# Performance work log

Hardware: AMD Instinct MI355X
Metric: run time of the kernel (lower is better)

Reference implementation:

```python
import jax, jax.numpy as jnp
import numpy as np

EMBD_DIM = 512
HIDDEN_DIM = 512
TARGET_DIM = 128
BATCH = 64
MAX_SET = 2048


def setup_inputs() -> dict:
    key = jax.random.key(0)
    ks = jax.random.split(key, 10)
    E, H, T = EMBD_DIM, HIDDEN_DIM, TARGET_DIM
    s = lambda fan_in: 1.0 / np.sqrt(fan_in)
    return {
        "words": jax.random.normal(ks[0], (BATCH, MAX_SET, E), dtype=jnp.float32),
        # attention_layer: Linear(2E -> H) followed by tanh; v: (H, 1)
        "W_att": jax.random.uniform(ks[1], (2 * E, H), jnp.float32, -s(2 * E), s(2 * E)),
        "b_att": jax.random.uniform(ks[2], (H,), jnp.float32, -s(2 * E), s(2 * E)),
        "v": jax.random.normal(ks[3], (H, 1), dtype=jnp.float32),
        # pred_net: Linear(E,H) -> ReLU -> Linear(H,H) -> ReLU -> Linear(H,T)
        "W1": jax.random.uniform(ks[4], (E, H), jnp.float32, -s(E), s(E)),
        "b1": jax.random.uniform(ks[5], (H,), jnp.float32, -s(E), s(E)),
        "W2": jax.random.uniform(ks[6], (H, H), jnp.float32, -s(H), s(H)),
        "b2": jax.random.uniform(ks[7], (H,), jnp.float32, -s(H), s(H)),
        "W3": jax.random.uniform(ks[8], (H, T), jnp.float32, -s(H), s(H)),
        "b3": jax.random.uniform(ks[9], (T,), jnp.float32, -s(H), s(H)),
    }


def reference(words, W_att, b_att, v, W1, b1, W2, b2, W3, b3):
    # words: [B, S, E]. A row is "valid" iff its feature-sum is nonzero
    # (matches words.sum(2).abs().sign() in the torch code).
    mask = jnp.sign(jnp.abs(words.sum(-1)))           # [B, S], 0/1 float
    lengths = mask.sum(axis=1, keepdims=True)          # [B, 1]
    # context = mean over valid rows (padded rows are exactly zero)
    context = words.sum(axis=1, keepdims=True) / lengths[..., None]  # [B, 1, E]
    context = jnp.broadcast_to(context, words.shape)   # [B, S, E]

    x = jnp.concatenate([words, context], axis=-1)     # [B, S, 2E]
    h = jnp.tanh(x @ W_att + b_att)                    # [B, S, H]
    scores = (h @ v)[..., 0]                           # [B, S]

    # per-segment softmax over valid rows only (masked_select + per-batch
    # Softmax in the original == masked softmax here)
    scores = jnp.where(mask > 0, scores, jnp.full_like(scores, -1e30))
    attn = jax.nn.softmax(scores, axis=1)              # [B, S]

    rep = jnp.einsum("bs,bse->be", attn, words)        # [B, E]

    pred = jax.nn.relu(rep @ W1 + b1)
    pred = jax.nn.relu(pred @ W2 + b2)
    pred = pred @ W3 + b3                              # [B, T]
    return pred
```

## Files before the change

### kernel.cpp

```cpp
#include <hip/hip_runtime.h>
#include <hip/hip_bf16.h>
#include <hip/hip_fp16.h>
#include <math.h>

#define B 64
#define S 2048
#define E 512
#define HD 512
#define TD 128
#define M_TOT (B*S)

#define OFF_MASK   0
#define OFF_CTXP   (OFF_MASK + B*S)
#define OFF_LENP   (OFF_CTXP + 8*B*E)
#define OFF_CB     (OFF_LENP + 8*B)
#define OFF_REPP   (OFF_CB + B*HD)
#define OFF_SC     (OFF_REPP + 8*B*E)
#define OFF_WPK    (OFF_SC + B*S)

typedef __attribute__((ext_vector_type(8))) short short8;
typedef __attribute__((ext_vector_type(4))) float f32x4;

__device__ inline unsigned int f2hu(float x) {
    __half h = __float2half(x);
    unsigned short u; __builtin_memcpy(&u, &h, 2); return (unsigned int)u;
}

__device__ inline float fast_tanh(float x) {
    float a = fabsf(x);
    float e = __expf(-2.0f * a);
    float r = (1.0f - e) / (1.0f + e);
    return copysignf(r, x);
}

__global__ __launch_bounds__(256)
void k0_pack(const float* __restrict__ W_att, unsigned short* __restrict__ Wpk)
{
    int tid = blockIdx.x*256 + threadIdx.x;
    int e = tid >> 9, h = tid & 511;
    float w = W_att[(size_t)e*HD + h];
    int kstep = e >> 5, kb = (e >> 3) & 3, j = e & 7, f = h >> 4, l15 = h & 15;
    size_t dst = ((((size_t)kstep*32 + f)*64) + kb*16 + l15)*8 + j;
    Wpk[dst] = (unsigned short)f2hu(w);
}

__global__ __launch_bounds__(256)
void k1_maskcol(const float* __restrict__ words, float* __restrict__ mask,
                float* __restrict__ ctxp, float* __restrict__ lenp)
{
    int bid = blockIdx.x;
    int b = bid >> 3, ch = bid & 7;
    int t = threadIdx.x;
    int w = t >> 6, l = t & 63;
    __shared__ __align__(16) float colred[4][E];
    __shared__ float lenred[4];
    const float* base = words + (size_t)(b * S + ch * 256) * E;
    float4 c0 = make_float4(0.f,0.f,0.f,0.f), c1 = make_float4(0.f,0.f,0.f,0.f);
    float wlen = 0.0f;
    for (int r = w; r < 256; r += 4) {
        const float* row = base + (size_t)r * E;
        float4 a  = *(const float4*)(row + 4*l);
        float4 bb = *(const float4*)(row + 256 + 4*l);
        float rs = a.x+a.y+a.z+a.w + bb.x+bb.y+bb.z+bb.w;
        #pragma unroll
        for (int m = 1; m < 64; m <<= 1) rs += __shfl_xor(rs, m);
        c0.x += a.x;  c0.y += a.y;  c0.z += a.z;  c0.w += a.w;
        c1.x += bb.x; c1.y += bb.y; c1.z += bb.z; c1.w += bb.w;
        if (l == 0) {
            float mv = (rs != 0.0f) ? 1.0f : 0.0f;
            mask[(size_t)b*S + ch*256 + r] = mv;
            wlen += mv;
        }
    }
    *(float4*)&colred[w][4*l]       = c0;
    *(float4*)&colred[w][256 + 4*l] = c1;
    if (l == 0) lenred[w] = wlen;
    __syncthreads();
    float s1 = colred[0][t]+colred[1][t]+colred[2][t]+colred[3][t];
    float s2 = colred[0][t+256]+colred[1][t+256]+colred[2][t+256]+colred[3][t+256];
    size_t o = ((size_t)ch * B + b) * E;
    ctxp[o + t]       = s1;
    ctxp[o + t + 256] = s2;
    if (t == 0) lenp[ch*B + b] = lenred[0]+lenred[1]+lenred[2]+lenred[3];
}

__global__ __launch_bounds__(256)
void k2_cb(const float* __restrict__ W_att, const float* __restrict__ b_att,
           const float* __restrict__ ctxp, const float* __restrict__ lenp,
           float* __restrict__ cb)
{
    int bid = blockIdx.x;
    int b = bid >> 1, hc = bid & 1;
    int t = threadIdx.x;
    __shared__ float ctxL[E];
    float len = 0.f;
    #pragma unroll
    for (int k = 0; k < 8; ++k) len += lenp[k*B + b];
    float inv = 1.0f / len;
    for (int c = t; c < E; c += 256) {
        float sv = 0.f;
        #pragma unroll
        for (int k = 0; k < 8; ++k) sv += ctxp[((size_t)k*B + b)*E + c];
        ctxL[c] = sv * inv;
    }
    __syncthreads();
    int h = hc*256 + t;
    const float* Wb = W_att + (size_t)E * HD;
    float a0 = b_att[h], a1 = 0.f, a2 = 0.f, a3 = 0.f;
    #pragma unroll 4
    for (int e = 0; e < E; e += 4) {
        a0 += ctxL[e]   * Wb[(size_t)e*HD + h];
        a1 += ctxL[e+1] * Wb[(size_t)(e+1)*HD + h];
        a2 += ctxL[e+2] * Wb[(size_t)(e+2)*HD + h];
        a3 += ctxL[e+3] * Wb[(size_t)(e+3)*HD + h];
    }
    cb[(size_t)b*HD + h] = (a0 + a1) + (a2 + a3);
}

__global__ __launch_bounds__(512, 3)
void k3_scores(const float* __restrict__ words,
               const unsigned short* __restrict__ Wpk,
               const float* __restrict__ cb, const float* __restrict__ v,
               float* __restrict__ sc)
{
    __shared__ __align__(16) unsigned char smem[16384];
    int mt = blockIdx.x;
    int m0 = mt * 64;
    int b  = m0 >> 11;
    int t = threadIdx.x;
    int lane = t & 63, wid = t >> 6;
    int wr = wid >> 2, wc = wid & 3;

    f32x4 acc[2][8];
    #pragma unroll
    for (int i = 0; i < 2; ++i)
        #pragma unroll
        for (int j = 0; j < 8; ++j) acc[i][j] = (f32x4)0.0f;

    {
    }
    int sks = t >> 8, sF = (t >> 6) & 3, skb = (t >> 4) & 3, sl15 = t & 15;
    int srow = sF*16 + sl15;
    const float* aSrc = words + (size_t)(m0 + srow)*E + sks*32 + skb*8;

    const unsigned short* bBase = Wpk + (((size_t)(wc*8))*64 + lane)*8;
#define LDB(kst,cf) (*(const short8*)(bBase + ((size_t)(kst)*32 + (cf))*512))

    float4 pa0, pa1, qa0, qa1;
#define LOADA(P0, P1, s) do { const float* _s = aSrc + (s)*64; \
        P0 = *(const float4*)(_s); P1 = *(const float4*)(_s + 4); } while(0)
#define STAGEA(buf, P0, P1) do { \
        unsigned int u0 = f2hu(P0.x) | (f2hu(P0.y) << 16); \
        unsigned int u1 = f2hu(P0.z) | (f2hu(P0.w) << 16); \
        unsigned int u2 = f2hu(P1.x) | (f2hu(P1.y) << 16); \
        unsigned int u3 = f2hu(P1.z) | (f2hu(P1.w) << 16); \
        *(uint4*)&(buf)[t*16] = make_uint4(u0, u1, u2, u3); } while(0)

    unsigned char* sm0 = smem;
    unsigned char* sm1 = smem + 8192;

    LOADA(pa0, pa1, 0);
    STAGEA(sm0, pa0, pa1);
    LOADA(pa0, pa1, 1);
    LOADA(qa0, qa1, 2);
    short8 bcur[8];
    #pragma unroll
    for (int cf = 0; cf < 8; ++cf) bcur[cf] = LDB(0, cf);
    __syncthreads();

#define KSUB(kst, BUFC, ksub) do { \
        short8 ah0 = *(const short8*)&(BUFC)[(ksub)*4096 + (wr*2    )*1024 + lane*16]; \
        short8 ah1 = *(const short8*)&(BUFC)[(ksub)*4096 + (wr*2 + 1)*1024 + lane*16]; \
        _Pragma("unroll") \
        for (int cf = 0; cf < 8; ++cf) { \
            acc[0][cf] = __builtin_amdgcn_mfma_f32_16x16x32_f16(ah0, bcur[cf], acc[0][cf], 0, 0, 0); \
            acc[1][cf] = __builtin_amdgcn_mfma_f32_16x16x32_f16(ah1, bcur[cf], acc[1][cf], 0, 0, 0); \
            if ((kst) < 15) bcur[cf] = LDB((kst) + 1, cf); \
        } } while(0)

#define SBODY(s, BUFC, BUFN, P0, P1) do { \
        if ((s) < 7) STAGEA(BUFN, P0, P1); \
        if ((s) < 5) LOADA(P0, P1, (s) + 3); \
        KSUB(2*(s),     BUFC, 0); \
        KSUB(2*(s) + 1, BUFC, 1); \
        __syncthreads(); } while(0)

    SBODY(0, sm0, sm1, pa0, pa1);
    SBODY(1, sm1, sm0, qa0, qa1);
    SBODY(2, sm0, sm1, pa0, pa1);
    SBODY(3, sm1, sm0, qa0, qa1);
    SBODY(4, sm0, sm1, pa0, pa1);
    SBODY(5, sm1, sm0, qa0, qa1);
    SBODY(6, sm0, sm1, pa0, pa1);
    SBODY(7, sm1, sm0, qa0, qa1);
#undef SBODY
#undef KSUB
#undef LOADA
#undef STAGEA
#undef LDB

    float ssum[2][4];
    #pragma unroll
    for (int i = 0; i < 2; ++i)
        #pragma unroll
        for (int rr = 0; rr < 4; ++rr) ssum[i][rr] = 0.f;

    #pragma unroll
    for (int cf = 0; cf < 8; ++cf) {
        int col = wc*128 + cf*16 + (lane & 15);
        float cbv = cb[(size_t)b*HD + col];
        float vv  = v[col];
        #pragma unroll
        for (int rf = 0; rf < 2; ++rf)
            #pragma unroll
            for (int rr = 0; rr < 4; ++rr)
                ssum[rf][rr] += fast_tanh(acc[rf][cf][rr] + cbv) * vv;
    }
    #pragma unroll
    for (int m = 1; m < 16; m <<= 1)
        #pragma unroll
        for (int rf = 0; rf < 2; ++rf)
            #pragma unroll
            for (int rr = 0; rr < 4; ++rr)
                ssum[rf][rr] += __shfl_xor(ssum[rf][rr], m);

    float* scr = (float*)smem;
    if ((lane & 15) == 0) {
        #pragma unroll
        for (int rf = 0; rf < 2; ++rf)
            #pragma unroll
            for (int rr = 0; rr < 4; ++rr)
                scr[wc*64 + wr*32 + rf*16 + (lane >> 4)*4 + rr] = ssum[rf][rr];
    }
    __syncthreads();
    if (t < 64) {
        float val = (scr[t] + scr[64 + t]) + (scr[128 + t] + scr[192 + t]);
        sc[(size_t)m0 + t] = val;
    }
}

__global__ __launch_bounds__(256)
void k4_rep(const float* __restrict__ words, const float* __restrict__ sc,
            const float* __restrict__ mask, float* __restrict__ repp)
{
    int bid = blockIdx.x;
    int b = bid >> 3, ch = bid & 7;
    int t = threadIdx.x;
    __shared__ float red[256];
    __shared__ float wrow[256];

    float xs[8];
    float mx = -1e30f;
    #pragma unroll
    for (int k = 0; k < 8; ++k) {
        size_t m = (size_t)b*S + 256*k + t;
        float x = sc[m];
        x = (mask[m] > 0.0f) ? x : -1e30f;
        xs[k] = x; mx = fmaxf(mx, x);
    }
    red[t] = mx; __syncthreads();
    for (int off = 128; off > 0; off >>= 1) {
        if (t < off) red[t] = fmaxf(red[t], red[t+off]);
        __syncthreads();
    }
    float gmax = red[0]; __syncthreads();
    float se = 0.f;
    #pragma unroll
    for (int k = 0; k < 8; ++k) se += expf(xs[k] - gmax);
    red[t] = se; __syncthreads();
    for (int off = 128; off > 0; off >>= 1) {
        if (t < off) red[t] += red[t+off];
        __syncthreads();
    }
    float den = red[0];
    wrow[t] = expf(xs[ch] - gmax) / den;
    __syncthreads();

    const float* base = words + (size_t)(b*S + ch*256)*E + 2*t;
    float2 acc = make_float2(0.f, 0.f);
    #pragma unroll 4
    for (int rr = 0; rr < 256; ++rr) {
        float2 wv = *(const float2*)(base + (size_t)rr*E);
        float a = wrow[rr];
        acc.x = fmaf(a, wv.x, acc.x);
        acc.y = fmaf(a, wv.y, acc.y);
    }
    size_t o = ((size_t)ch*B + b)*E + 2*t;
    *(float2*)&repp[o] = acc;
}

__global__ __launch_bounds__(256)
void k5_mlp(const float* __restrict__ repp,
            const float* __restrict__ W1, const float* __restrict__ b1,
            const float* __restrict__ W2, const float* __restrict__ b2,
            const float* __restrict__ W3, const float* __restrict__ b3,
            float* __restrict__ out)
{
    int b = blockIdx.x;
    int t = threadIdx.x;
    __shared__ float xL[HD];
    __shared__ float yL[HD];
    for (int c = t; c < E; c += 256) {
        float sv = 0.f;
        #pragma unroll
        for (int k = 0; k < 8; ++k) sv += repp[((size_t)k*B + b)*E + c];
        xL[c] = sv;
    }
    __syncthreads();
    #pragma unroll
    for (int oo = 0; oo < 2; ++oo) {
        int h = oo*256 + t;
        float a0 = b1[h], a1 = 0.f, a2 = 0.f, a3 = 0.f;
        #pragma unroll 4
        for (int e = 0; e < E; e += 4) {
            a0 += xL[e]   * W1[(size_t)e*HD + h];
            a1 += xL[e+1] * W1[(size_t)(e+1)*HD + h];
            a2 += xL[e+2] * W1[(size_t)(e+2)*HD + h];
            a3 += xL[e+3] * W1[(size_t)(e+3)*HD + h];
        }
        yL[h] = fmaxf((a0 + a1) + (a2 + a3), 0.f);
    }
    __syncthreads();
    float l2v[2];
    #pragma unroll
    for (int oo = 0; oo < 2; ++oo) {
        int h = oo*256 + t;
        float a0 = b2[h], a1 = 0.f, a2 = 0.f, a3 = 0.f;
        #pragma unroll 4
        for (int e = 0; e < HD; e += 4) {
            a0 += yL[e]   * W2[(size_t)e*HD + h];
            a1 += yL[e+1] * W2[(size_t)(e+1)*HD + h];
            a2 += yL[e+2] * W2[(size_t)(e+2)*HD + h];
            a3 += yL[e+3] * W2[(size_t)(e+3)*HD + h];
        }
        l2v[oo] = fmaxf((a0 + a1) + (a2 + a3), 0.f);
    }
    __syncthreads();
    xL[t] = l2v[0]; xL[256 + t] = l2v[1];
    __syncthreads();
    if (t < TD) {
        float a0 = b3[t], a1 = 0.f, a2 = 0.f, a3 = 0.f;
        #pragma unroll 4
        for (int e = 0; e < HD; e += 4) {
            a0 += xL[e]   * W3[(size_t)e*TD + t];
            a1 += xL[e+1] * W3[(size_t)(e+1)*TD + t];
            a2 += xL[e+2] * W3[(size_t)(e+2)*TD + t];
            a3 += xL[e+3] * W3[(size_t)(e+3)*TD + t];
        }
        out[(size_t)b*TD + t] = (a0 + a1) + (a2 + a3);
    }
}

extern "C" void kernel_launch(void* const* d_in, const int* in_sizes, int n_in,
                              void* d_out, int out_size, void* d_ws, size_t ws_size,
                              hipStream_t stream)
{
    const float* words = (const float*)d_in[0];
    const float* W_att = (const float*)d_in[1];
    const float* b_att = (const float*)d_in[2];
    const float* v     = (const float*)d_in[3];
    const float* W1    = (const float*)d_in[4];
    const float* b1    = (const float*)d_in[5];
    const float* W2    = (const float*)d_in[6];
    const float* b2    = (const float*)d_in[7];
    const float* W3    = (const float*)d_in[8];
    const float* b3    = (const float*)d_in[9];
    (void)in_sizes; (void)n_in; (void)out_size; (void)ws_size;

    float* ws   = (float*)d_ws;
    float* mask = ws + OFF_MASK;
    float* ctxp = ws + OFF_CTXP;
    float* lenp = ws + OFF_LENP;
    float* cb   = ws + OFF_CB;
    float* repp = ws + OFF_REPP;
    float* sc   = ws + OFF_SC;
    unsigned short* Wpk = (unsigned short*)(ws + OFF_WPK);
    float* out  = (float*)d_out;

    hipLaunchKernelGGL(k0_pack,    dim3(1024), dim3(256), 0, stream, W_att, Wpk);
    hipLaunchKernelGGL(k1_maskcol, dim3(B*8),  dim3(256), 0, stream, words, mask, ctxp, lenp);
    hipLaunchKernelGGL(k2_cb,      dim3(B*2),  dim3(256), 0, stream, W_att, b_att, ctxp, lenp, cb);
    hipLaunchKernelGGL(k3_scores,  dim3(2048), dim3(512), 0, stream, words, Wpk, cb, v, sc);
    hipLaunchKernelGGL(k4_rep,     dim3(B*8),  dim3(256), 0, stream, words, sc, mask, repp);
    hipLaunchKernelGGL(k5_mlp,     dim3(B),    dim3(256), 0, stream, repp, W1, b1, W2, b2, W3, b3, out);
}
```

Baseline: 358.7 us.

## Double M-tile of score GEMM to 128 rows with double-buffered B fragments

The scores kernel now processes 128 rows per block instead of 64, so each wave holds 4 row fragments and reuses every loaded W_att fragment across twice as many MFMAs. This halves the global reads of the packed weight matrix. The K loop is restructured into 16 steps of 32, with ping-pong B register buffers prefetched one step ahead. In exchange the kernel uses more accumulator registers, occupancy drops to 2 blocks per CU, and there are more barriers per tile.

After: 322.1 us. 10.2% less time.

```diff
diff --git a/kernel.cpp b/kernel.cpp
--- a/kernel.cpp
+++ b/kernel.cpp
@@ -117,7 +117,7 @@
     cb[(size_t)b*HD + h] = (a0 + a1) + (a2 + a3);
 }
 
-__global__ __launch_bounds__(512, 3)
+__global__ __launch_bounds__(512, 2)
 void k3_scores(const float* __restrict__ words,
                const unsigned short* __restrict__ Wpk,
                const float* __restrict__ cb, const float* __restrict__ v,
@@ -125,29 +125,27 @@
 {
     __shared__ __align__(16) unsigned char smem[16384];
     int mt = blockIdx.x;
-    int m0 = mt * 64;
+    int m0 = mt * 128;
     int b  = m0 >> 11;
     int t = threadIdx.x;
     int lane = t & 63, wid = t >> 6;
     int wr = wid >> 2, wc = wid & 3;
 
-    f32x4 acc[2][8];
-    #pragma unroll
-    for (int i = 0; i < 2; ++i)
+    f32x4 acc[4][8];
+    #pragma unroll
+    for (int i = 0; i < 4; ++i)
         #pragma unroll
         for (int j = 0; j < 8; ++j) acc[i][j] = (f32x4)0.0f;
 
-    {
-    }
-    int sks = t >> 8, sF = (t >> 6) & 3, skb = (t >> 4) & 3, sl15 = t & 15;
+    int sF = (t >> 6) & 7, skb = (t >> 4) & 3, sl15 = t & 15;
     int srow = sF*16 + sl15;
-    const float* aSrc = words + (size_t)(m0 + srow)*E + sks*32 + skb*8;
+    const float* aSrc = words + (size_t)(m0 + srow)*E + skb*8;
 
     const unsigned short* bBase = Wpk + (((size_t)(wc*8))*64 + lane)*8;
 #define LDB(kst,cf) (*(const short8*)(bBase + ((size_t)(kst)*32 + (cf))*512))
 
     float4 pa0, pa1, qa0, qa1;
-#define LOADA(P0, P1, s) do { const float* _s = aSrc + (s)*64; \
+#define LOADA(P0, P1, s) do { const float* _s = aSrc + (s)*32; \
         P0 = *(const float4*)(_s); P1 = *(const float4*)(_s + 4); } while(0)
 #define STAGEA(buf, P0, P1) do { \
         unsigned int u0 = f2hu(P0.x) | (f2hu(P0.y) << 16); \
@@ -159,49 +157,59 @@
     unsigned char* sm0 = smem;
     unsigned char* sm1 = smem + 8192;
 
+    short8 bA[8], bB[8];
+
     LOADA(pa0, pa1, 0);
     STAGEA(sm0, pa0, pa1);
     LOADA(pa0, pa1, 1);
     LOADA(qa0, qa1, 2);
-    short8 bcur[8];
-    #pragma unroll
-    for (int cf = 0; cf < 8; ++cf) bcur[cf] = LDB(0, cf);
-    __syncthreads();
-
-#define KSUB(kst, BUFC, ksub) do { \
-        short8 ah0 = *(const short8*)&(BUFC)[(ksub)*4096 + (wr*2    )*1024 + lane*16]; \
-        short8 ah1 = *(const short8*)&(BUFC)[(ksub)*4096 + (wr*2 + 1)*1024 + lane*16]; \
+    #pragma unroll
+    for (int cf = 0; cf < 8; ++cf) bA[cf] = LDB(0, cf);
+    __syncthreads();
+
+#define KBODY(k, BUFC, BUFN, P0, P1, BCUR, BNEXT) do { \
+        short8 ah[4]; \
+        _Pragma("unroll") \
+        for (int rf = 0; rf < 4; ++rf) \
+            ah[rf] = *(const short8*)&(BUFC)[(wr*4 + rf)*1024 + lane*16]; \
+        if ((k) < 15) { \
+            _Pragma("unroll") \
+            for (int cf = 0; cf < 8; ++cf) BNEXT[cf] = LDB((k)+1, cf); \
+            STAGEA(BUFN, P0, P1); \
+        } \
+        if ((k) < 13) LOADA(P0, P1, (k) + 3); \
         _Pragma("unroll") \
         for (int cf = 0; cf < 8; ++cf) { \
-            acc[0][cf] = __builtin_amdgcn_mfma_f32_16x16x32_f16(ah0, bcur[cf], acc[0][cf], 0, 0, 0); \
-            acc[1][cf] = __builtin_amdgcn_mfma_f32_16x16x32_f16(ah1, bcur[cf], acc[1][cf], 0, 0, 0); \
-            if ((kst) < 15) bcur[cf] = LDB((kst) + 1, cf); \
-        } } while(0)
-
-#define SBODY(s, BUFC, BUFN, P0, P1) do { \
-        if ((s) < 7) STAGEA(BUFN, P0, P1); \
-        if ((s) < 5) LOADA(P0, P1, (s) + 3); \
-        KSUB(2*(s),     BUFC, 0); \
-        KSUB(2*(s) + 1, BUFC, 1); \
+            _Pragma("unroll") \
+            for (int rf = 0; rf < 4; ++rf) \
+                acc[rf][cf] = __builtin_amdgcn_mfma_f32_16x16x32_f16(ah[rf], BCUR[cf], acc[rf][cf], 0, 0, 0); \
+        } \
         __syncthreads(); } while(0)
 
-    SBODY(0, sm0, sm1, pa0, pa1);
-    SBODY(1, sm1, sm0, qa0, qa1);
-    SBODY(2, sm0, sm1, pa0, pa1);
-    SBODY(3, sm1, sm0, qa0, qa1);
-    SBODY(4, sm0, sm1, pa0, pa1);
-    SBODY(5, sm1, sm0, qa0, qa1);
-    SBODY(6, sm0, sm1, pa0, pa1);
-    SBODY(7, sm1, sm0, qa0, qa1);
-#undef SBODY
-#undef KSUB
+    KBODY( 0, sm0, sm1, pa0, pa1, bA, bB);
+    KBODY( 1, sm1, sm0, qa0, qa1, bB, bA);
+    KBODY( 2, sm0, sm1, pa0, pa1, bA, bB);
+    KBODY( 3, sm1, sm0, qa0, qa1, bB, bA);
+    KBODY( 4, sm0, sm1, pa0, pa1, bA, bB);
+    KBODY( 5, sm1, sm0, qa0, qa1, bB, bA);
+    KBODY( 6, sm0, sm1, pa0, pa1, bA, bB);
+    KBODY( 7, sm1, sm0, qa0, qa1, bB, bA);
+    KBODY( 8, sm0, sm1, pa0, pa1, bA, bB);
+    KBODY( 9, sm1, sm0, qa0, qa1, bB, bA);
+    KBODY(10, sm0, sm1, pa0, pa1, bA, bB);
+    KBODY(11, sm1, sm0, qa0, qa1, bB, bA);
+    KBODY(12, sm0, sm1, pa0, pa1, bA, bB);
+    KBODY(13, sm1, sm0, qa0, qa1, bB, bA);
+    KBODY(14, sm0, sm1, pa0, pa1, bA, bB);
+    KBODY(15, sm1, sm0, qa0, qa1, bB, bA);
+#undef KBODY
 #undef LOADA
 #undef STAGEA
 #undef LDB
 
-    float ssum[2][4];
-    #pragma unroll
-    for (int i = 0; i < 2; ++i)
+    float ssum[4][4];
+    #pragma unroll
+    for (int i = 0; i < 4; ++i)
         #pragma unroll
         for (int rr = 0; rr < 4; ++rr) ssum[i][rr] = 0.f;
 
@@ -211,7 +219,7 @@
         float cbv = cb[(size_t)b*HD + col];
         float vv  = v[col];
         #pragma unroll
-        for (int rf = 0; rf < 2; ++rf)
+        for (int rf = 0; rf < 4; ++rf)
             #pragma unroll
             for (int rr = 0; rr < 4; ++rr)
                 ssum[rf][rr] += fast_tanh(acc[rf][cf][rr] + cbv) * vv;
@@ -219,7 +227,7 @@
     #pragma unroll
     for (int m = 1; m < 16; m <<= 1)
         #pragma unroll
-        for (int rf = 0; rf < 2; ++rf)
+        for (int rf = 0; rf < 4; ++rf)
             #pragma unroll
             for (int rr = 0; rr < 4; ++rr)
                 ssum[rf][rr] += __shfl_xor(ssum[rf][rr], m);
@@ -227,14 +235,14 @@
     float* scr = (float*)smem;
     if ((lane & 15) == 0) {
         #pragma unroll
-        for (int rf = 0; rf < 2; ++rf)
+        for (int rf = 0; rf < 4; ++rf)
             #pragma unroll
             for (int rr = 0; rr < 4; ++rr)
-                scr[wc*64 + wr*32 + rf*16 + (lane >> 4)*4 + rr] = ssum[rf][rr];
-    }
-    __syncthreads();
-    if (t < 64) {
-        float val = (scr[t] + scr[64 + t]) + (scr[128 + t] + scr[192 + t]);
+                scr[wc*128 + wr*64 + rf*16 + (lane >> 4)*4 + rr] = ssum[rf][rr];
+    }
+    __syncthreads();
+    if (t < 128) {
+        float val = (scr[t] + scr[128 + t]) + (scr[256 + t] + scr[384 + t]);
         sc[(size_t)m0 + t] = val;
     }
 }
@@ -380,7 +388,7 @@
     hipLaunchKernelGGL(k0_pack,    dim3(1024), dim3(256), 0, stream, W_att, Wpk);
     hipLaunchKernelGGL(k1_maskcol, dim3(B*8),  dim3(256), 0, stream, words, mask, ctxp, lenp);
     hipLaunchKernelGGL(k2_cb,      dim3(B*2),  dim3(256), 0, stream, W_att, b_att, ctxp, lenp, cb);
-    hipLaunchKernelGGL(k3_scores,  dim3(2048), dim3(512), 0, stream, words, Wpk, cb, v, sc);
+    hipLaunchKernelGGL(k3_scores,  dim3(1024), dim3(512), 0, stream, words, Wpk, cb, v, sc);
     hipLaunchKernelGGL(k4_rep,     dim3(B*8),  dim3(256), 0, stream, words, sc, mask, repp);
     hipLaunchKernelGGL(k5_mlp,     dim3(B),    dim3(256), 0, stream, repp, W1, b1, W2, b2, W3, b3, out);
 }
```
